# Kernel optimization log

Hardware: AMD Instinct MI355X
Metric: run time of the kernel (lower is better)

The kernel has to match this reference:

```python
import jax, jax.numpy as jnp
import numpy as np

B, T, D = 64, 2048, 300

def setup_inputs() -> dict:
    key = jax.random.key(0)
    k1, k2, k3, k4 = jax.random.split(key, 4)
    gate_encoding = jax.random.uniform(k1, (B, T, D), dtype=jnp.float32)
    inputs_encoding = jax.random.normal(k2, (B, T, D), dtype=jnp.float32)
    # kaiming-normal-ish init: std = sqrt(2 / fan_in)
    std = float(np.sqrt(2.0 / D))
    Wz = jax.random.normal(k3, (D, D), dtype=jnp.float32) * std
    Wo = jax.random.normal(k4, (D, D), dtype=jnp.float32) * std
    bz = jnp.zeros((D,), dtype=jnp.float32)
    bo = jnp.zeros((D,), dtype=jnp.float32)
    return {"gate_encoding": gate_encoding, "inputs_encoding": inputs_encoding,
            "Wz": Wz, "bz": bz, "Wo": Wo, "bo": bo}

def reference(gate_encoding, inputs_encoding, Wz, bz, Wo, bo):
    # Batch the two linear projections across all timesteps (torch.nn.Linear: x @ W.T + b)
    z = jnp.tanh(jnp.einsum('btd,ed->bte', inputs_encoding, Wz) + bz)  # [B,T,D]
    o = jnp.tanh(jnp.einsum('btd,ed->bte', inputs_encoding, Wo) + bo)  # [B,T,D]

    # Sequential gated recurrence: c_t = g_t * c_{t-1} + (1 - g_t) * z_t ; h_t = o_t * c_t
    def step(c, gz_o):
        g_t, z_t, o_t = gz_o
        c = g_t * c + (1.0 - g_t) * z_t
        return c, o_t * c

    c0 = jnp.zeros((gate_encoding.shape[0], gate_encoding.shape[2]), dtype=inputs_encoding.dtype)
    # scan over time: move T to leading axis
    _, h = jax.lax.scan(step, c0,
                        (jnp.swapaxes(gate_encoding, 0, 1),
                         jnp.swapaxes(z, 0, 1),
                         jnp.swapaxes(o, 0, 1)))
    return jnp.swapaxes(h, 0, 1)  # [B,T,D]
```

## Files before the change

### kernel.cpp

```cpp
#include <hip/hip_runtime.h>
#include <hip/hip_bf16.h>

typedef _Float16 f16x8 __attribute__((ext_vector_type(8)));
typedef _Float16 f16x4 __attribute__((ext_vector_type(4)));
typedef float f32x4 __attribute__((ext_vector_type(4)));

#define B_SZ 64
#define T_SZ 2048
#define D_SZ 300
#define M_SZ (B_SZ * T_SZ)
#define KP 320
#define NP 640
#define NCHUNK 32
#define CLEN 64

__device__ __forceinline__ void gld_lds16(const void* g, void* l) {
    __builtin_amdgcn_global_load_lds(
        (const __attribute__((address_space(1))) unsigned int*)g,
        (__attribute__((address_space(3))) unsigned int*)l,
        16, 0, 0);
}

__device__ __forceinline__ float fast_tanh(float x) {
    float e = __expf(2.0f * x);
    return 1.0f - 2.0f * __builtin_amdgcn_rcpf(e + 1.0f);
}

__global__ void pack_w(const float* __restrict__ Wz, const float* __restrict__ Wo,
                       _Float16* __restrict__ W) {
    unsigned int i = blockIdx.x * 256u + threadIdx.x;
    if (i >= NP * KP) return;
    unsigned int n = i / KP;
    unsigned int k = i - n * KP;
    float v = 0.0f;
    if (k < D_SZ) {
        if (n < D_SZ) v = Wz[n * D_SZ + k];
        else if (n >= 320 && n < 320 + D_SZ) v = Wo[(n - 320) * D_SZ + k];
    }
    W[i] = (_Float16)v;
}

__global__ void pack_bias(const float* __restrict__ bz, const float* __restrict__ bo,
                          float* __restrict__ bias, float* __restrict__ zpad) {
    int n = threadIdx.x;
    float v = 0.0f;
    if (n < D_SZ) v = bz[n];
    else if (n >= 320 && n < 320 + D_SZ) v = bo[n - 320];
    bias[n] = v;
    if (n < 16) zpad[n] = 0.0f;
}

__device__ __forceinline__ f16x8 cvt8(f32x4 v0, f32x4 v1) {
    f16x8 r;
    r[0] = (_Float16)v0[0]; r[1] = (_Float16)v0[1];
    r[2] = (_Float16)v0[2]; r[3] = (_Float16)v0[3];
    r[4] = (_Float16)v1[0]; r[5] = (_Float16)v1[1];
    r[6] = (_Float16)v1[2]; r[7] = (_Float16)v1[3];
    return r;
}

__global__ __launch_bounds__(256) void gemm_zo(const float* __restrict__ X,
                                               const _Float16* __restrict__ W,
                                               const float* __restrict__ bias,
                                               const float* __restrict__ zpad,
                                               _Float16* __restrict__ C) {
    __shared__ float    As[2][128 * 32];
    __shared__ _Float16 Bs[2][128 * 32];

    const int tid = threadIdx.x;
    const int lane = tid & 63;
    const int wid = tid >> 6;
    const int wm = wid >> 1, wn = wid & 1;

    int g = blockIdx.x;
    int s = (g & 7) * (5120 / 8) + (g >> 3);
    int bm = s / 5;
    int bn = s - bm * 5;

    const int l15 = lane & 15;
    const int kq = lane >> 4;

    f32x4 acc[4][4] = {};

    const int arow_in = lane >> 3;
    const int asrc_u = (lane & 7) ^ arow_in;
    const int brow_in = lane >> 2;
    const int bsrc_u = (lane & 3) ^ ((brow_in >> 1) & 3);

    auto stage = [&](int buf, int kt) {
#pragma unroll
        for (int j = 0; j < 4; ++j) {
            int c = wid * 4 + j;
            int row = c * 8 + arow_in;
            const float* src = (kt == 9 && asrc_u >= 3)
                ? zpad
                : X + (size_t)(bm * 128 + row) * D_SZ + kt * 32 + asrc_u * 4;
            gld_lds16(src, &As[buf][c * 256]);
        }
#pragma unroll
        for (int j = 0; j < 2; ++j) {
            int c = wid + j * 4;
            int row = c * 16 + brow_in;
            gld_lds16(W + (size_t)(bn * 128 + row) * KP + kt * 32 + bsrc_u * 8,
                      &Bs[buf][c * 512]);
        }
    };

    stage(0, 0);
    __syncthreads();

    int buf = 0;
#pragma unroll 1
    for (int kt = 0; kt < 10; ++kt) {
        if (kt < 9) stage(buf ^ 1, kt + 1);

        const int key = l15 & 7;
        f16x8 bf[4], af[4];
#pragma unroll
        for (int ns = 0; ns < 4; ++ns) {
            int row = wn * 64 + ns * 16 + l15;
            int u = kq ^ ((row >> 1) & 3);
            bf[ns] = *(const f16x8*)&Bs[buf][row * 32 + u * 8];
        }
#pragma unroll
        for (int ms = 0; ms < 4; ++ms) {
            int row = wm * 64 + ms * 16 + l15;
            f32x4 lo = *(const f32x4*)&As[buf][row * 32 + ((kq * 2 + 0) ^ key) * 4];
            f32x4 hi = *(const f32x4*)&As[buf][row * 32 + ((kq * 2 + 1) ^ key) * 4];
            af[ms] = cvt8(lo, hi);
        }

        __builtin_amdgcn_s_setprio(1);
#pragma unroll
        for (int ms = 0; ms < 4; ++ms)
#pragma unroll
            for (int ns = 0; ns < 4; ++ns)
                acc[ms][ns] = __builtin_amdgcn_mfma_f32_16x16x32_f16(bf[ns], af[ms], acc[ms][ns], 0, 0, 0);
        __builtin_amdgcn_s_setprio(0);

        __syncthreads();
        buf ^= 1;
    }

    const int mrow0 = bm * 128 + wm * 64;
    const int ncol0 = bn * 128 + wn * 64;
    _Float16* et = (_Float16*)&As[0][0] + wid * 1024;
    const int key = l15 & 7;

    f32x4 b4[4];
#pragma unroll
    for (int ns = 0; ns < 4; ++ns)
        b4[ns] = *(const f32x4*)&bias[ncol0 + ns * 16 + kq * 4];

#pragma unroll
    for (int ms = 0; ms < 4; ++ms) {
#pragma unroll
        for (int ns = 0; ns < 4; ++ns) {
            f16x4 v;
#pragma unroll
            for (int r = 0; r < 4; ++r)
                v[r] = (_Float16)fast_tanh(acc[ms][ns][r] + b4[ns][r]);
            int u = (ns * 2 + (kq >> 1)) ^ key;
            *(f16x4*)&et[l15 * 64 + u * 8 + (kq & 1) * 4] = v;
        }
        int m = mrow0 + ms * 16 + l15;
#pragma unroll
        for (int j = 0; j < 2; ++j) {
            int ur = j * 4 + kq;
            f16x8 o = *(const f16x8*)&et[l15 * 64 + (ur ^ key) * 8];
            *(f16x8*)&C[(size_t)m * NP + ncol0 + ur * 8] = o;
        }
    }
}

__global__ void scan_p1(const float* __restrict__ gate, const _Float16* __restrict__ C,
                        float* __restrict__ Aout, float* __restrict__ Bout) {
    int b = blockIdx.x >> 5;
    int nc = blockIdx.x & 31;
    int d = threadIdx.x;
    if (d >= D_SZ) return;
    size_t base = (size_t)b * T_SZ + (size_t)nc * CLEN;
    const float* gp = gate + base * D_SZ + d;
    const _Float16* zp = C + base * NP + d;
    float A = 1.0f, Bc = 0.0f;
    for (int t = 0; t < CLEN; ++t) {
        float gv = gp[(size_t)t * D_SZ];
        float zv = (float)zp[(size_t)t * NP];
        A *= gv;
        Bc = gv * Bc + (1.0f - gv) * zv;
    }
    int o = (b * NCHUNK + nc) * D_SZ + d;
    Aout[o] = A;
    Bout[o] = Bc;
}

__global__ void scan_p2(const float* __restrict__ A, const float* __restrict__ Bc,
                        float* __restrict__ Cin) {
    int idx = blockIdx.x * 256 + threadIdx.x;
    if (idx >= B_SZ * D_SZ) return;
    int b = idx / D_SZ;
    int d = idx - b * D_SZ;
    float c = 0.0f;
    for (int nc = 0; nc < NCHUNK; ++nc) {
        int o = (b * NCHUNK + nc) * D_SZ + d;
        Cin[o] = c;
        c = A[o] * c + Bc[o];
    }
}

__global__ void scan_p3(const float* __restrict__ gate, const _Float16* __restrict__ C,
                        const float* __restrict__ Cin, float* __restrict__ out) {
    int b = blockIdx.x >> 5;
    int nc = blockIdx.x & 31;
    int d = threadIdx.x;
    if (d >= D_SZ) return;
    size_t base = (size_t)b * T_SZ + (size_t)nc * CLEN;
    const float* gp = gate + base * D_SZ + d;
    const _Float16* zp = C + base * NP + d;
    const _Float16* op = zp + 320;
    float* hp = out + base * D_SZ + d;
    float c = Cin[(b * NCHUNK + nc) * D_SZ + d];
    for (int t = 0; t < CLEN; ++t) {
        float gv = gp[(size_t)t * D_SZ];
        float zv = (float)zp[(size_t)t * NP];
        float ov = (float)op[(size_t)t * NP];
        c = gv * c + (1.0f - gv) * zv;
        hp[(size_t)t * D_SZ] = ov * c;
    }
}

extern "C" void kernel_launch(void* const* d_in, const int* in_sizes, int n_in,
                              void* d_out, int out_size, void* d_ws, size_t ws_size,
                              hipStream_t stream) {
    const float* gate = (const float*)d_in[0];
    const float* xin  = (const float*)d_in[1];
    const float* Wz   = (const float*)d_in[2];
    const float* bz   = (const float*)d_in[3];
    const float* Wo   = (const float*)d_in[4];
    const float* bo   = (const float*)d_in[5];
    float* out = (float*)d_out;

    char* ws = (char*)d_ws;
    _Float16* C16  = (_Float16*)(ws);
    _Float16* Wc   = (_Float16*)(ws + 167772160ull);
    float*    bias = (float*)   (ws + 168181760ull);
    float*    zpad = (float*)   (ws + 168184320ull);
    float*    Ach  = (float*)   (ws + 168184576ull);
    float*    Bch  = (float*)   (ws + 170642176ull);
    float*    Cin  = (float*)   (ws + 173099776ull);

    pack_w<<<(NP * KP + 255) / 256, 256, 0, stream>>>(Wz, Wo, Wc);
    pack_bias<<<1, NP, 0, stream>>>(bz, bo, bias, zpad);

    gemm_zo<<<(M_SZ / 128) * (NP / 128), 256, 0, stream>>>(xin, Wc, bias, zpad, C16);

    scan_p1<<<B_SZ * NCHUNK, 320, 0, stream>>>(gate, C16, Ach, Bch);
    scan_p2<<<(B_SZ * D_SZ + 255) / 256, 256, 0, stream>>>(Ach, Bch, Cin);
    scan_p3<<<B_SZ * NCHUNK, 320, 0, stream>>>(gate, C16, Cin, out);
}
```

Before: 306.6 us.

## Stage A tile through registers as fp16 and store epilogue directly

The GEMM now loads the fp32 input tile into registers, converts it to fp16, and writes it to shared memory after the MFMA loop. This replaces the direct global-to-LDS fp32 copy followed by per-iteration conversion, halving A's LDS footprint and removing the zero-pad buffer. The epilogue writes f16x4 results straight to global memory instead of going through an LDS transpose, and launch bounds now request 4 blocks per CU. The trade-off is more register pressure from holding the prefetched A data, and narrower, less coalesced output stores.

```diff
diff --git a/kernel.cpp b/kernel.cpp
--- a/kernel.cpp
+++ b/kernel.cpp
@@ -41,13 +41,12 @@
 }
 
 __global__ void pack_bias(const float* __restrict__ bz, const float* __restrict__ bo,
-                          float* __restrict__ bias, float* __restrict__ zpad) {
+                          float* __restrict__ bias) {
     int n = threadIdx.x;
     float v = 0.0f;
     if (n < D_SZ) v = bz[n];
     else if (n >= 320 && n < 320 + D_SZ) v = bo[n - 320];
     bias[n] = v;
-    if (n < 16) zpad[n] = 0.0f;
 }
 
 __device__ __forceinline__ f16x8 cvt8(f32x4 v0, f32x4 v1) {
@@ -59,12 +58,11 @@
     return r;
 }
 
-__global__ __launch_bounds__(256) void gemm_zo(const float* __restrict__ X,
-                                               const _Float16* __restrict__ W,
-                                               const float* __restrict__ bias,
-                                               const float* __restrict__ zpad,
-                                               _Float16* __restrict__ C) {
-    __shared__ float    As[2][128 * 32];
+__global__ __launch_bounds__(256, 4) void gemm_zo(const float* __restrict__ X,
+                                                  const _Float16* __restrict__ W,
+                                                  const float* __restrict__ bias,
+                                                  _Float16* __restrict__ C) {
+    __shared__ _Float16 As[2][128 * 32];
     __shared__ _Float16 Bs[2][128 * 32];
 
     const int tid = threadIdx.x;
@@ -82,21 +80,17 @@
 
     f32x4 acc[4][4] = {};
 
-    const int arow_in = lane >> 3;
-    const int asrc_u = (lane & 7) ^ arow_in;
+    const int ar = tid >> 1;
+    const int au = (tid & 1) * 2;
+    const float* asrc = X + (size_t)(bm * 128 + ar) * D_SZ;
+    const int aswz = (ar >> 1) & 3;
+    _Float16* adst0 = &As[0][ar * 32 + (au ^ aswz) * 8];
+    _Float16* adst1 = &As[0][ar * 32 + ((au + 1) ^ aswz) * 8];
+
     const int brow_in = lane >> 2;
     const int bsrc_u = (lane & 3) ^ ((brow_in >> 1) & 3);
 
-    auto stage = [&](int buf, int kt) {
-#pragma unroll
-        for (int j = 0; j < 4; ++j) {
-            int c = wid * 4 + j;
-            int row = c * 8 + arow_in;
-            const float* src = (kt == 9 && asrc_u >= 3)
-                ? zpad
-                : X + (size_t)(bm * 128 + row) * D_SZ + kt * 32 + asrc_u * 4;
-            gld_lds16(src, &As[buf][c * 256]);
-        }
+    auto stageB = [&](int buf, int kt) {
 #pragma unroll
         for (int j = 0; j < 2; ++j) {
             int c = wid + j * 4;
@@ -106,15 +100,38 @@
         }
     };
 
-    stage(0, 0);
+    f32x4 av[4];
+    auto loadA = [&](int kt) {
+        int k0 = kt * 32 + au * 8;
+        if (kt < 9) {
+#pragma unroll
+            for (int j = 0; j < 4; ++j) av[j] = *(const f32x4*)(asrc + k0 + j * 4);
+        } else {
+#pragma unroll
+            for (int j = 0; j < 4; ++j) {
+                int k = k0 + j * 4;
+                av[j] = (k < D_SZ) ? *(const f32x4*)(asrc + k) : f32x4{};
+            }
+        }
+    };
+    auto writeA = [&](int buf) {
+        *(f16x8*)(adst0 + buf * 128 * 32) = cvt8(av[0], av[1]);
+        *(f16x8*)(adst1 + buf * 128 * 32) = cvt8(av[2], av[3]);
+    };
+
+    loadA(0);
+    stageB(0, 0);
+    writeA(0);
     __syncthreads();
 
     int buf = 0;
 #pragma unroll 1
     for (int kt = 0; kt < 10; ++kt) {
-        if (kt < 9) stage(buf ^ 1, kt + 1);
-
-        const int key = l15 & 7;
+        if (kt < 9) {
+            loadA(kt + 1);
+            stageB(buf ^ 1, kt + 1);
+        }
+
         f16x8 bf[4], af[4];
 #pragma unroll
         for (int ns = 0; ns < 4; ++ns) {
@@ -125,9 +142,8 @@
 #pragma unroll
         for (int ms = 0; ms < 4; ++ms) {
             int row = wm * 64 + ms * 16 + l15;
-            f32x4 lo = *(const f32x4*)&As[buf][row * 32 + ((kq * 2 + 0) ^ key) * 4];
-            f32x4 hi = *(const f32x4*)&As[buf][row * 32 + ((kq * 2 + 1) ^ key) * 4];
-            af[ms] = cvt8(lo, hi);
+            int u = kq ^ ((row >> 1) & 3);
+            af[ms] = *(const f16x8*)&As[buf][row * 32 + u * 8];
         }
 
         __builtin_amdgcn_s_setprio(1);
@@ -138,37 +154,26 @@
                 acc[ms][ns] = __builtin_amdgcn_mfma_f32_16x16x32_f16(bf[ns], af[ms], acc[ms][ns], 0, 0, 0);
         __builtin_amdgcn_s_setprio(0);
 
+        if (kt < 9) writeA(buf ^ 1);
+
         __syncthreads();
         buf ^= 1;
     }
 
     const int mrow0 = bm * 128 + wm * 64;
     const int ncol0 = bn * 128 + wn * 64;
-    _Float16* et = (_Float16*)&As[0][0] + wid * 1024;
-    const int key = l15 & 7;
-
-    f32x4 b4[4];
-#pragma unroll
-    for (int ns = 0; ns < 4; ++ns)
-        b4[ns] = *(const f32x4*)&bias[ncol0 + ns * 16 + kq * 4];
-
-#pragma unroll
-    for (int ms = 0; ms < 4; ++ms) {
-#pragma unroll
-        for (int ns = 0; ns < 4; ++ns) {
+#pragma unroll
+    for (int ns = 0; ns < 4; ++ns) {
+        int nb = ncol0 + ns * 16 + kq * 4;
+        f32x4 b4 = *(const f32x4*)&bias[nb];
+#pragma unroll
+        for (int ms = 0; ms < 4; ++ms) {
+            int m = mrow0 + ms * 16 + l15;
             f16x4 v;
 #pragma unroll
             for (int r = 0; r < 4; ++r)
-                v[r] = (_Float16)fast_tanh(acc[ms][ns][r] + b4[ns][r]);
-            int u = (ns * 2 + (kq >> 1)) ^ key;
-            *(f16x4*)&et[l15 * 64 + u * 8 + (kq & 1) * 4] = v;
-        }
-        int m = mrow0 + ms * 16 + l15;
-#pragma unroll
-        for (int j = 0; j < 2; ++j) {
-            int ur = j * 4 + kq;
-            f16x8 o = *(const f16x8*)&et[l15 * 64 + (ur ^ key) * 8];
-            *(f16x8*)&C[(size_t)m * NP + ncol0 + ur * 8] = o;
+                v[r] = (_Float16)fast_tanh(acc[ms][ns][r] + b4[r]);
+            *(f16x4*)&C[(size_t)m * NP + nb] = v;
         }
     }
 }
@@ -244,15 +249,14 @@
     _Float16* C16  = (_Float16*)(ws);
     _Float16* Wc   = (_Float16*)(ws + 167772160ull);
     float*    bias = (float*)   (ws + 168181760ull);
-    float*    zpad = (float*)   (ws + 168184320ull);
-    float*    Ach  = (float*)   (ws + 168184576ull);
-    float*    Bch  = (float*)   (ws + 170642176ull);
-    float*    Cin  = (float*)   (ws + 173099776ull);
+    float*    Ach  = (float*)   (ws + 168184320ull);
+    float*    Bch  = (float*)   (ws + 170641920ull);
+    float*    Cin  = (float*)   (ws + 173099520ull);
 
     pack_w<<<(NP * KP + 255) / 256, 256, 0, stream>>>(Wz, Wo, Wc);
-    pack_bias<<<1, NP, 0, stream>>>(bz, bo, bias, zpad);
-
-    gemm_zo<<<(M_SZ / 128) * (NP / 128), 256, 0, stream>>>(xin, Wc, bias, zpad, C16);
+    pack_bias<<<1, NP, 0, stream>>>(bz, bo, bias);
+
+    gemm_zo<<<(M_SZ / 128) * (NP / 128), 256, 0, stream>>>(xin, Wc, bias, C16);
 
     scan_p1<<<B_SZ * NCHUNK, 320, 0, stream>>>(gate, C16, Ach, Bch);
     scan_p2<<<(B_SZ * D_SZ + 255) / 256, 256, 0, stream>>>(Ach, Bch, Cin);
```

Result: slower. 341.5 us (+11.4%).
